# Optimization experiments

Hardware: AMD Instinct MI355X
Metric: run time of the kernel (lower is better)

The kernel has to match this reference:

```python
import jax, jax.numpy as jnp
import numpy as np

B, S, D = 4, 2048, 768
H = 12
HD = D // H  # 64
SCALE = HD ** -0.5

def setup_inputs() -> dict:
    key = jax.random.key(0)
    k1, k2, k3 = jax.random.split(key, 3)
    x = jax.random.normal(k1, (B, S, D), dtype=jnp.float32)
    w_qkv = jax.random.normal(k2, (D, 3 * D), dtype=jnp.float32) * (D ** -0.5)
    w_out = jax.random.normal(k3, (D, D), dtype=jnp.float32) * (D ** -0.5)
    b_out = jnp.zeros((D,), dtype=jnp.float32)
    return {"x": x, "w_qkv": w_qkv, "w_out": w_out, "b_out": b_out}

def reference(x, w_qkv, w_out, b_out):
    B_, S_, D_ = x.shape
    # qkv projection (no bias), then 'b s (qkv h d) -> qkv b h s d'
    qkv = (x @ w_qkv).reshape(B_, S_, 3, H, HD).transpose(2, 0, 3, 1, 4)
    q, k, v = qkv[0], qkv[1], qkv[2]  # each [B, H, S, HD]
    att = jnp.einsum('bhxd,bhyd->bhxy', q, k) * SCALE
    att = jax.nn.softmax(att, axis=-1)  # dropout_rate=0 -> identity
    out = jnp.einsum('bhxy,bhyd->bhxd', att, v)
    out = out.transpose(0, 2, 1, 3).reshape(B_, S_, D_)  # 'b h s d -> b s (h d)'
    return out @ w_out + b_out
```

## Files before the change

kernel.cpp:

```cpp
#include <hip/hip_runtime.h>

#define BB 4
#define SS 2048
#define DD 768
#define HH 12
#define HDIM 64

using bf16_t = __bf16;
typedef __bf16 bf16x8 __attribute__((ext_vector_type(8)));
typedef __bf16 bf16x4 __attribute__((ext_vector_type(4)));
typedef __bf16 bf16x2 __attribute__((ext_vector_type(2)));
typedef float f32x4 __attribute__((ext_vector_type(4)));
typedef float f32x16 __attribute__((ext_vector_type(16)));
typedef unsigned int u32;
typedef unsigned int u32x4 __attribute__((ext_vector_type(4)));

static __device__ __forceinline__ void cp16(void* lds, const void* g) {
  __builtin_amdgcn_global_load_lds(
      (const __attribute__((address_space(1))) u32*)g,
      (__attribute__((address_space(3))) u32*)lds, 16, 0, 0);
}

__global__ void cvt_x(const float* __restrict__ in, bf16_t* __restrict__ out) {
  const size_t i = ((size_t)blockIdx.x * 256 + threadIdx.x) * 8;
  f32x4 f0 = *(const f32x4*)(in + i);
  f32x4 f1 = *(const f32x4*)(in + i + 4);
  bf16x8 v;
#pragma unroll
  for (int j = 0; j < 4; j++) { v[j] = (bf16_t)f0[j]; v[4 + j] = (bf16_t)f1[j]; }
  *(bf16x8*)(out + i) = v;
}

__global__ void wt_transpose(const float* __restrict__ in, bf16_t* __restrict__ out,
                             int K, int N) {
  __shared__ bf16_t tile[64][65];
  const int n0 = blockIdx.x * 64, k0 = blockIdx.y * 64;
  const int t = threadIdx.x;
  const int r = t >> 2;
  const int c0 = (t & 3) * 16;
  const float* src = in + (size_t)(k0 + r) * N + n0 + c0;
#pragma unroll
  for (int q = 0; q < 4; q++) {
    f32x4 f = *(const f32x4*)(src + q * 4);
#pragma unroll
    for (int j = 0; j < 4; j++) tile[r][c0 + q * 4 + j] = (bf16_t)f[j];
  }
  __syncthreads();
  bf16x8 o0, o1;
#pragma unroll
  for (int j = 0; j < 8; j++) { o0[j] = tile[c0 + j][r]; o1[j] = tile[c0 + 8 + j][r]; }
  *(bf16x8*)(out + (size_t)(n0 + r) * K + k0 + c0) = o0;
  *(bf16x8*)(out + (size_t)(n0 + r) * K + k0 + c0 + 8) = o1;
}

template <int MODE>
__global__ __launch_bounds__(256, 2)
void gemm_bt(const bf16_t* __restrict__ A, const bf16_t* __restrict__ Bt,
             int M, int N, int K,
             bf16_t* __restrict__ q_out, bf16_t* __restrict__ k_out,
             bf16_t* __restrict__ vt_out,
             float* __restrict__ Cout, const float* __restrict__ bias) {
  __shared__ bf16_t As[2][128][64];
  __shared__ bf16_t Bs[2][128][64];
  const int t = threadIdx.x;
  const int lane = t & 63, wave = t >> 6;
  const int l15 = lane & 15, quad = lane >> 4;
  const int wm = (wave >> 1) * 64, wn = (wave & 1) * 64;

  const int nx = gridDim.x;
  const int L = blockIdx.y * nx + blockIdx.x;
  const int chunk = (nx * gridDim.y) >> 3;
  const int v = (L & 7) * chunk + (L >> 3);
  const int m0 = (v / nx) * 128, n0 = (v % nx) * 128;

  const int srow = lane >> 3;
  const int schunk = ((lane & 7) ^ srow) * 8;
  const int rsw = l15 & 7;

  f32x4 acc[4][4];
#pragma unroll
  for (int i = 0; i < 4; i++)
#pragma unroll
    for (int j = 0; j < 4; j++) acc[i][j] = (f32x4){0.f, 0.f, 0.f, 0.f};

  auto stage = [&](int k0, int buf) {
#pragma unroll
    for (int p = 0; p < 4; p++) {
      const int row = wave * 32 + p * 8 + srow;
      const bf16_t* asrc;
      if (MODE == 0) {
        asrc = A + (size_t)(m0 + row) * K + k0 + schunk;
      } else {
        const int mm = m0 + row, b = mm >> 11, s = mm & 2047, h = k0 >> 6;
        asrc = A + (((size_t)(b * HH + h)) * SS + s) * HDIM + schunk;
      }
      cp16(&As[buf][wave * 32 + p * 8][0], asrc);
      cp16(&Bs[buf][wave * 32 + p * 8][0],
           Bt + (size_t)(n0 + row) * K + k0 + schunk);
    }
  };

  const int NT = K / 64;
  stage(0, 0);

  for (int kt = 0; kt < NT; kt++) {
    const int buf = kt & 1;
    __syncthreads();
    if (kt + 1 < NT) stage((kt + 1) * 64, buf ^ 1);
#pragma unroll
    for (int kk = 0; kk < 2; kk++) {
      bf16x8 af[4], bfr[4];
#pragma unroll
      for (int i = 0; i < 4; i++)
        af[i] = *(const bf16x8*)&As[buf][wm + i * 16 + l15][((kk * 4 + quad) ^ rsw) * 8];
#pragma unroll
      for (int j = 0; j < 4; j++)
        bfr[j] = *(const bf16x8*)&Bs[buf][wn + j * 16 + l15][((kk * 4 + quad) ^ rsw) * 8];
#pragma unroll
      for (int i = 0; i < 4; i++)
#pragma unroll
        for (int j = 0; j < 4; j++)
          acc[i][j] = __builtin_amdgcn_mfma_f32_16x16x32_bf16(af[i], bfr[j], acc[i][j], 0, 0, 0);
    }
  }

  const float QSCALE = 0.125f * 1.44269504088896340736f;
#pragma unroll
  for (int i = 0; i < 4; i++) {
    const int mbase = m0 + wm + i * 16 + quad * 4;
#pragma unroll
    for (int j = 0; j < 4; j++) {
      const int n = n0 + wn + j * 16 + l15;
#pragma unroll
      for (int r = 0; r < 4; r++) {
        const float v = acc[i][j][r];
        const int mm = mbase + r;
        if (MODE == 0) {
          const int sel = n / DD;
          const int rem = n - sel * DD;
          const int h = rem >> 6, d = rem & 63;
          const int b = mm >> 11, s = mm & 2047;
          if (sel == 2) {
            vt_out[((size_t)(b * HH + h) * HDIM + d) * SS + s] = (bf16_t)v;
          } else {
            const size_t idx = (((size_t)(b * HH + h)) * SS + s) * HDIM + d;
            if (sel == 0) q_out[idx] = (bf16_t)(v * QSCALE);
            else k_out[idx] = (bf16_t)v;
          }
        } else {
          Cout[(size_t)mm * N + n] = v + bias[n];
        }
      }
    }
  }
}

__global__ __launch_bounds__(256, 3)
void attn_kernel(bf16_t* __restrict__ Qio, const bf16_t* __restrict__ Kg,
                 const bf16_t* __restrict__ Vt) {
  __shared__ bf16_t Ks[2][64][64];
  __shared__ bf16_t Vts[2][64][64];
  __shared__ float lsum[128];
  const int t = threadIdx.x;
  const int lane = t & 63, wave = t >> 6;
  const int l31 = lane & 31, hi = lane >> 5;

  const int L = blockIdx.y * gridDim.x + blockIdx.x;
  const int v = (L & 7) * ((16 * BB * HH) / 8) + (L >> 3);
  const int bh = v >> 4;
  const int q0 = (v & 15) * 128;

  const size_t base = (size_t)bh * SS * HDIM;
  const size_t baset = (size_t)bh * HDIM * SS;
  const int wq = wave * 32;
  const int srow = lane >> 3;
  const int schunk = ((lane & 7) ^ srow) * 8;
  const int rsw = l31 & 7;

  bf16x8 qf[4];
#pragma unroll
  for (int kd = 0; kd < 4; kd++)
    qf[kd] = *(const bf16x8*)(Qio + base + (size_t)(q0 + wq + l31) * HDIM +
                              kd * 16 + hi * 8);

  float l_lane = 0.f;
  f32x16 o_acc[2];
#pragma unroll
  for (int dt = 0; dt < 2; dt++)
#pragma unroll
    for (int r = 0; r < 16; r++) o_acc[dt][r] = 0.f;

  f32x16 sA[2], sB[2];

  auto stageK = [&](int k0, int buf) {
#pragma unroll
    for (int p = 0; p < 2; p++)
      cp16(&Ks[buf][wave * 16 + p * 8][0],
           Kg + base + (size_t)(k0 + wave * 16 + p * 8 + srow) * HDIM + schunk);
  };
  auto stageV = [&](int k0, int buf) {
#pragma unroll
    for (int p = 0; p < 2; p++)
      cp16(&Vts[buf][wave * 16 + p * 8][0],
           Vt + baset + (size_t)(wave * 16 + p * 8 + srow) * SS + k0 + schunk);
  };

  auto qk = [&](int buf, f32x16 (&s)[2]) {
    __builtin_amdgcn_s_setprio(1);
#pragma unroll
    for (int ct = 0; ct < 2; ct++) {
#pragma unroll
      for (int r = 0; r < 16; r++) s[ct][r] = 0.f;
#pragma unroll
      for (int kd = 0; kd < 4; kd++) {
        bf16x8 kf = *(const bf16x8*)&Ks[buf][ct * 32 + l31][((2 * kd + hi) ^ rsw) * 8];
        s[ct] = __builtin_amdgcn_mfma_f32_32x32x16_bf16(kf, qf[kd], s[ct], 0, 0, 0);
      }
    }
    __builtin_amdgcn_s_setprio(0);
  };

  auto smpv = [&](int buf, const f32x16 (&sT)[2]) {
    bf16x8 pa[4];
#pragma unroll
    for (int ct = 0; ct < 2; ct++) {
      float p[16];
#pragma unroll
      for (int r = 0; r < 16; r++) p[r] = __builtin_amdgcn_exp2f(sT[ct][r]);
#pragma unroll
      for (int r = 0; r < 16; r += 4)
        l_lane += (p[r] + p[r + 1]) + (p[r + 2] + p[r + 3]);
      u32 w[4][2];
#pragma unroll
      for (int g = 0; g < 4; g++)
#pragma unroll
        for (int i = 0; i < 2; i++) {
          bf16x2 pk = {(bf16_t)p[4 * g + 2 * i], (bf16_t)p[4 * g + 2 * i + 1]};
          w[g][i] = *(u32*)&pk;
        }
#pragma unroll
      for (int sub = 0; sub < 2; sub++) {
        u32 a0 = w[2 * sub][0], b0 = w[2 * sub + 1][0];
        u32 a1 = w[2 * sub][1], b1 = w[2 * sub + 1][1];
        asm volatile("v_permlane32_swap_b32 %0, %1" : "+v"(a0), "+v"(b0));
        asm volatile("v_permlane32_swap_b32 %0, %1" : "+v"(a1), "+v"(b1));
        u32x4 fr = {a0, a1, b0, b1};
        pa[ct * 2 + sub] = *(bf16x8*)&fr;
      }
    }
    __builtin_amdgcn_s_setprio(1);
#pragma unroll
    for (int kk = 0; kk < 4; kk++)
#pragma unroll
      for (int dt = 0; dt < 2; dt++) {
        bf16x8 vf = *(const bf16x8*)&Vts[buf][dt * 32 + l31][((2 * kk + hi) ^ rsw) * 8];
        o_acc[dt] = __builtin_amdgcn_mfma_f32_32x32x16_bf16(pa[kk], vf, o_acc[dt], 0, 0, 0);
      }
    __builtin_amdgcn_s_setprio(0);
  };

  stageK(0, 0); stageK(64, 1); stageV(0, 0);
  __syncthreads();
  qk(0, sA);
  __syncthreads();

#pragma unroll 1
  for (int it = 0; it < 30; it += 2) {
    stageK((it + 2) * 64, 0);
    stageV((it + 1) * 64, 1);
    qk(1, sB);
    smpv(0, sA);
    __syncthreads();
    stageK((it + 3) * 64, 1);
    stageV((it + 2) * 64, 0);
    qk(0, sA);
    smpv(1, sB);
    __syncthreads();
  }
  stageV(31 * 64, 1);
  qk(1, sB);
  smpv(0, sA);
  __syncthreads();
  smpv(1, sB);

  const float lf = l_lane + __shfl_xor(l_lane, 32);
  lsum[wq + l31] = lf;
#pragma unroll
  for (int r = 0; r < 16; r++) {
    const int q = wq + (r & 3) + 8 * (r >> 2) + 4 * hi;
    const float inv = 1.0f / lsum[q];
#pragma unroll
    for (int dt = 0; dt < 2; dt++) {
      const int d = dt * 32 + l31;
      Qio[base + (size_t)(q0 + q) * HDIM + d] = (bf16_t)(o_acc[dt][r] * inv);
    }
  }
}

extern "C" void kernel_launch(void* const* d_in, const int* in_sizes, int n_in,
                              void* d_out, int out_size, void* d_ws, size_t ws_size,
                              hipStream_t stream) {
  const float* x = (const float*)d_in[0];
  const float* w_qkv = (const float*)d_in[1];
  const float* w_out = (const float*)d_in[2];
  const float* b_out = (const float*)d_in[3];
  float* out = (float*)d_out;

  char* ws = (char*)d_ws;
  bf16_t* wqkv_t = (bf16_t*)ws; ws += (size_t)3 * DD * DD * 2;
  bf16_t* wout_t = (bf16_t*)ws; ws += (size_t)DD * DD * 2;
  bf16_t* q_ws = (bf16_t*)ws;   ws += (size_t)BB * HH * SS * HDIM * 2;
  bf16_t* k_ws = (bf16_t*)ws;
  bf16_t* vt_sc = (bf16_t*)d_out;
  bf16_t* xb = (bf16_t*)d_out + (size_t)BB * SS * DD;

  cvt_x<<<(BB * SS * DD) / (256 * 8), 256, 0, stream>>>(x, xb);
  wt_transpose<<<dim3(3 * DD / 64, DD / 64), 256, 0, stream>>>(w_qkv, wqkv_t, DD, 3 * DD);
  wt_transpose<<<dim3(DD / 64, DD / 64), 256, 0, stream>>>(w_out, wout_t, DD, DD);
  gemm_bt<0><<<dim3(3 * DD / 128, BB * SS / 128), 256, 0, stream>>>(
      xb, wqkv_t, BB * SS, 3 * DD, DD, q_ws, k_ws, vt_sc, nullptr, nullptr);
  attn_kernel<<<dim3(SS / 128, BB * HH), 256, 0, stream>>>(q_ws, k_ws, vt_sc);
  gemm_bt<1><<<dim3(DD / 128, BB * SS / 128), 256, 0, stream>>>(
      q_ws, wout_t, BB * SS, DD, DD, nullptr, nullptr, nullptr, out, b_out);
}
```

Baseline: 229.1 us.

## Halve GEMM K-tile to raise occupancy and change attention LDS swizzle

The GEMM kernel now stages 32-wide K slices instead of 64, halving LDS per block, and raises launch bounds so four blocks can fit per CU. The XOR swizzle on GEMM LDS reads is dropped, which may bring back bank conflicts, and the loop now does twice as many iterations and barriers. The attention kernel's K/V staging gets a different XOR swizzle that mixes in the row group, aimed at cutting LDS bank conflicts when the 32x32 MFMA fragments are read.

Result: slower. 246.2 us (+7.5%).

```diff
diff --git a/kernel.cpp b/kernel.cpp
--- a/kernel.cpp
+++ b/kernel.cpp
@@ -54,14 +54,14 @@
 }
 
 template <int MODE>
-__global__ __launch_bounds__(256, 2)
+__global__ __launch_bounds__(256, 4)
 void gemm_bt(const bf16_t* __restrict__ A, const bf16_t* __restrict__ Bt,
              int M, int N, int K,
              bf16_t* __restrict__ q_out, bf16_t* __restrict__ k_out,
              bf16_t* __restrict__ vt_out,
              float* __restrict__ Cout, const float* __restrict__ bias) {
-  __shared__ bf16_t As[2][128][64];
-  __shared__ bf16_t Bs[2][128][64];
+  __shared__ bf16_t As[2][128][32];
+  __shared__ bf16_t Bs[2][128][32];
   const int t = threadIdx.x;
   const int lane = t & 63, wave = t >> 6;
   const int l15 = lane & 15, quad = lane >> 4;
@@ -73,9 +73,8 @@
   const int v = (L & 7) * chunk + (L >> 3);
   const int m0 = (v / nx) * 128, n0 = (v % nx) * 128;
 
-  const int srow = lane >> 3;
-  const int schunk = ((lane & 7) ^ srow) * 8;
-  const int rsw = l15 & 7;
+  const int drow = lane >> 2;
+  const int dcol = (lane & 3) * 8;
 
   f32x4 acc[4][4];
 #pragma unroll
@@ -85,43 +84,40 @@
 
   auto stage = [&](int k0, int buf) {
 #pragma unroll
-    for (int p = 0; p < 4; p++) {
-      const int row = wave * 32 + p * 8 + srow;
+    for (int c = 0; c < 2; c++) {
+      const int row = wave * 32 + c * 16 + drow;
       const bf16_t* asrc;
       if (MODE == 0) {
-        asrc = A + (size_t)(m0 + row) * K + k0 + schunk;
+        asrc = A + (size_t)(m0 + row) * K + k0 + dcol;
       } else {
         const int mm = m0 + row, b = mm >> 11, s = mm & 2047, h = k0 >> 6;
-        asrc = A + (((size_t)(b * HH + h)) * SS + s) * HDIM + schunk;
-      }
-      cp16(&As[buf][wave * 32 + p * 8][0], asrc);
-      cp16(&Bs[buf][wave * 32 + p * 8][0],
-           Bt + (size_t)(n0 + row) * K + k0 + schunk);
-    }
-  };
-
-  const int NT = K / 64;
+        asrc = A + (((size_t)(b * HH + h)) * SS + s) * HDIM + (k0 & 63) + dcol;
+      }
+      cp16(&As[buf][wave * 32 + c * 16][0], asrc);
+      cp16(&Bs[buf][wave * 32 + c * 16][0],
+           Bt + (size_t)(n0 + row) * K + k0 + dcol);
+    }
+  };
+
+  const int NT = K / 32;
   stage(0, 0);
 
   for (int kt = 0; kt < NT; kt++) {
     const int buf = kt & 1;
     __syncthreads();
-    if (kt + 1 < NT) stage((kt + 1) * 64, buf ^ 1);
-#pragma unroll
-    for (int kk = 0; kk < 2; kk++) {
-      bf16x8 af[4], bfr[4];
-#pragma unroll
-      for (int i = 0; i < 4; i++)
-        af[i] = *(const bf16x8*)&As[buf][wm + i * 16 + l15][((kk * 4 + quad) ^ rsw) * 8];
+    if (kt + 1 < NT) stage((kt + 1) * 32, buf ^ 1);
+    bf16x8 af[4], bfr[4];
+#pragma unroll
+    for (int i = 0; i < 4; i++)
+      af[i] = *(const bf16x8*)&As[buf][wm + i * 16 + l15][quad * 8];
+#pragma unroll
+    for (int j = 0; j < 4; j++)
+      bfr[j] = *(const bf16x8*)&Bs[buf][wn + j * 16 + l15][quad * 8];
+#pragma unroll
+    for (int i = 0; i < 4; i++)
 #pragma unroll
       for (int j = 0; j < 4; j++)
-        bfr[j] = *(const bf16x8*)&Bs[buf][wn + j * 16 + l15][((kk * 4 + quad) ^ rsw) * 8];
-#pragma unroll
-      for (int i = 0; i < 4; i++)
-#pragma unroll
-        for (int j = 0; j < 4; j++)
-          acc[i][j] = __builtin_amdgcn_mfma_f32_16x16x32_bf16(af[i], bfr[j], acc[i][j], 0, 0, 0);
-    }
+        acc[i][j] = __builtin_amdgcn_mfma_f32_16x16x32_bf16(af[i], bfr[j], acc[i][j], 0, 0, 0);
   }
 
   const float QSCALE = 0.125f * 1.44269504088896340736f;
@@ -174,8 +170,7 @@
   const size_t baset = (size_t)bh * HDIM * SS;
   const int wq = wave * 32;
   const int srow = lane >> 3;
-  const int schunk = ((lane & 7) ^ srow) * 8;
-  const int rsw = l31 & 7;
+  const int rsw = (l31 & 7) ^ (l31 >> 3);
 
   bf16x8 qf[4];
 #pragma unroll
@@ -194,15 +189,19 @@
 
   auto stageK = [&](int k0, int buf) {
 #pragma unroll
-    for (int p = 0; p < 2; p++)
+    for (int p = 0; p < 2; p++) {
+      const int sc = ((lane & 7) ^ srow ^ ((wave * 2 + p) & 3)) * 8;
       cp16(&Ks[buf][wave * 16 + p * 8][0],
-           Kg + base + (size_t)(k0 + wave * 16 + p * 8 + srow) * HDIM + schunk);
+           Kg + base + (size_t)(k0 + wave * 16 + p * 8 + srow) * HDIM + sc);
+    }
   };
   auto stageV = [&](int k0, int buf) {
 #pragma unroll
-    for (int p = 0; p < 2; p++)
+    for (int p = 0; p < 2; p++) {
+      const int sc = ((lane & 7) ^ srow ^ ((wave * 2 + p) & 3)) * 8;
       cp16(&Vts[buf][wave * 16 + p * 8][0],
-           Vt + baset + (size_t)(wave * 16 + p * 8 + srow) * SS + k0 + schunk);
+           Vt + baset + (size_t)(wave * 16 + p * 8 + srow) * SS + k0 + sc);
+    }
   };
 
   auto qk = [&](int buf, f32x16 (&s)[2]) {
```

## Use 256x256 tiles for QKV GEMM and add extra LDS swizzle in attention

Applied to the files above, without the earlier changes.

Splits the templated GEMM into a dedicated QKV kernel using 256x256 output tiles, 512 threads and a K-step of 32, plus a separate projection kernel. The larger tile raises arithmetic intensity per LDS load and cuts the block count to 288. The attention kernel's K/V staging gets an extra XOR term in its swizzle, aimed at fewer LDS bank conflicts. In exchange, the larger accumulator raises register pressure, the shorter K-step means more barriers per unit of work, and fewer blocks may balance poorly across CUs.

After: 262.8 us. 14.7% more time.

```diff
diff --git a/kernel.cpp b/kernel.cpp
--- a/kernel.cpp
+++ b/kernel.cpp
@@ -53,19 +53,101 @@
   *(bf16x8*)(out + (size_t)(n0 + r) * K + k0 + c0 + 8) = o1;
 }
 
-template <int MODE>
+__global__ __launch_bounds__(512, 2)
+void gemm_qkv(const bf16_t* __restrict__ A, const bf16_t* __restrict__ Bt,
+              bf16_t* __restrict__ q_out, bf16_t* __restrict__ k_out,
+              bf16_t* __restrict__ vt_out) {
+  __shared__ bf16_t As[2][256][32];
+  __shared__ bf16_t Bs[2][256][32];
+  const int t = threadIdx.x;
+  const int lane = t & 63, wave = t >> 6;
+  const int l15 = lane & 15, quad = lane >> 4;
+  const int wm = (wave >> 2) * 128, wn = (wave & 3) * 64;
+  const int K = DD;
+
+  const int L = blockIdx.y * 9 + blockIdx.x;
+  const int v = (L & 7) * 36 + (L >> 3);
+  const int m0 = (v / 9) * 256, n0 = (v % 9) * 256;
+
+  const int drow = lane >> 2;
+  const int dcol = ((lane & 3) ^ ((lane >> 3) & 3)) * 8;
+  const int rxor = (l15 >> 1) & 3;
+
+  f32x4 acc[8][4];
+#pragma unroll
+  for (int i = 0; i < 8; i++)
+#pragma unroll
+    for (int j = 0; j < 4; j++) acc[i][j] = (f32x4){0.f, 0.f, 0.f, 0.f};
+
+  auto stage = [&](int k0, int buf) {
+#pragma unroll
+    for (int c = 0; c < 2; c++) {
+      const int row = wave * 32 + c * 16 + drow;
+      cp16(&As[buf][wave * 32 + c * 16][0],
+           A + (size_t)(m0 + row) * K + k0 + dcol);
+      cp16(&Bs[buf][wave * 32 + c * 16][0],
+           Bt + (size_t)(n0 + row) * K + k0 + dcol);
+    }
+  };
+
+  const int NT = K / 32;
+  stage(0, 0);
+
+  for (int kt = 0; kt < NT; kt++) {
+    const int buf = kt & 1;
+    __syncthreads();
+    if (kt + 1 < NT) stage((kt + 1) * 32, buf ^ 1);
+    bf16x8 af[8], bfr[4];
+#pragma unroll
+    for (int i = 0; i < 8; i++)
+      af[i] = *(const bf16x8*)&As[buf][wm + i * 16 + l15][(quad ^ rxor) * 8];
+#pragma unroll
+    for (int j = 0; j < 4; j++)
+      bfr[j] = *(const bf16x8*)&Bs[buf][wn + j * 16 + l15][(quad ^ rxor) * 8];
+#pragma unroll
+    for (int i = 0; i < 8; i++)
+#pragma unroll
+      for (int j = 0; j < 4; j++)
+        acc[i][j] = __builtin_amdgcn_mfma_f32_16x16x32_bf16(af[i], bfr[j], acc[i][j], 0, 0, 0);
+  }
+
+  const float QSCALE = 0.125f * 1.44269504088896340736f;
+#pragma unroll
+  for (int i = 0; i < 8; i++) {
+    const int mbase = m0 + wm + i * 16 + quad * 4;
+#pragma unroll
+    for (int j = 0; j < 4; j++) {
+      const int n = n0 + wn + j * 16 + l15;
+#pragma unroll
+      for (int r = 0; r < 4; r++) {
+        const float v = acc[i][j][r];
+        const int mm = mbase + r;
+        const int sel = n / DD;
+        const int rem = n - sel * DD;
+        const int h = rem >> 6, d = rem & 63;
+        const int b = mm >> 11, s = mm & 2047;
+        if (sel == 2) {
+          vt_out[((size_t)(b * HH + h) * HDIM + d) * SS + s] = (bf16_t)v;
+        } else {
+          const size_t idx = (((size_t)(b * HH + h)) * SS + s) * HDIM + d;
+          if (sel == 0) q_out[idx] = (bf16_t)(v * QSCALE);
+          else k_out[idx] = (bf16_t)v;
+        }
+      }
+    }
+  }
+}
+
 __global__ __launch_bounds__(256, 2)
-void gemm_bt(const bf16_t* __restrict__ A, const bf16_t* __restrict__ Bt,
-             int M, int N, int K,
-             bf16_t* __restrict__ q_out, bf16_t* __restrict__ k_out,
-             bf16_t* __restrict__ vt_out,
-             float* __restrict__ Cout, const float* __restrict__ bias) {
+void gemm_proj(const bf16_t* __restrict__ A, const bf16_t* __restrict__ Bt,
+               float* __restrict__ Cout, const float* __restrict__ bias) {
   __shared__ bf16_t As[2][128][64];
   __shared__ bf16_t Bs[2][128][64];
   const int t = threadIdx.x;
   const int lane = t & 63, wave = t >> 6;
   const int l15 = lane & 15, quad = lane >> 4;
   const int wm = (wave >> 1) * 64, wn = (wave & 1) * 64;
+  const int K = DD, N = DD;
 
   const int nx = gridDim.x;
   const int L = blockIdx.y * nx + blockIdx.x;
@@ -87,14 +169,9 @@
 #pragma unroll
     for (int p = 0; p < 4; p++) {
       const int row = wave * 32 + p * 8 + srow;
-      const bf16_t* asrc;
-      if (MODE == 0) {
-        asrc = A + (size_t)(m0 + row) * K + k0 + schunk;
-      } else {
-        const int mm = m0 + row, b = mm >> 11, s = mm & 2047, h = k0 >> 6;
-        asrc = A + (((size_t)(b * HH + h)) * SS + s) * HDIM + schunk;
-      }
-      cp16(&As[buf][wave * 32 + p * 8][0], asrc);
+      const int mm = m0 + row, b = mm >> 11, s = mm & 2047, h = k0 >> 6;
+      cp16(&As[buf][wave * 32 + p * 8][0],
+           A + (((size_t)(b * HH + h)) * SS + s) * HDIM + schunk);
       cp16(&Bs[buf][wave * 32 + p * 8][0],
            Bt + (size_t)(n0 + row) * K + k0 + schunk);
     }
@@ -124,7 +201,6 @@
     }
   }
 
-  const float QSCALE = 0.125f * 1.44269504088896340736f;
 #pragma unroll
   for (int i = 0; i < 4; i++) {
     const int mbase = m0 + wm + i * 16 + quad * 4;
@@ -132,25 +208,8 @@
     for (int j = 0; j < 4; j++) {
       const int n = n0 + wn + j * 16 + l15;
 #pragma unroll
-      for (int r = 0; r < 4; r++) {
-        const float v = acc[i][j][r];
-        const int mm = mbase + r;
-        if (MODE == 0) {
-          const int sel = n / DD;
-          const int rem = n - sel * DD;
-          const int h = rem >> 6, d = rem & 63;
-          const int b = mm >> 11, s = mm & 2047;
-          if (sel == 2) {
-            vt_out[((size_t)(b * HH + h) * HDIM + d) * SS + s] = (bf16_t)v;
-          } else {
-            const size_t idx = (((size_t)(b * HH + h)) * SS + s) * HDIM + d;
-            if (sel == 0) q_out[idx] = (bf16_t)(v * QSCALE);
-            else k_out[idx] = (bf16_t)v;
-          }
-        } else {
-          Cout[(size_t)mm * N + n] = v + bias[n];
-        }
-      }
+      for (int r = 0; r < 4; r++)
+        Cout[(size_t)(mbase + r) * N + n] = acc[i][j][r] + bias[n];
     }
   }
 }
@@ -174,8 +233,7 @@
   const size_t baset = (size_t)bh * HDIM * SS;
   const int wq = wave * 32;
   const int srow = lane >> 3;
-  const int schunk = ((lane & 7) ^ srow) * 8;
-  const int rsw = l31 & 7;
+  const int rsw = (l31 & 7) ^ (l31 >> 3);
 
   bf16x8 qf[4];
 #pragma unroll
@@ -194,15 +252,19 @@
 
   auto stageK = [&](int k0, int buf) {
 #pragma unroll
-    for (int p = 0; p < 2; p++)
+    for (int p = 0; p < 2; p++) {
+      const int sc = ((lane & 7) ^ srow ^ ((wave * 2 + p) & 3)) * 8;
       cp16(&Ks[buf][wave * 16 + p * 8][0],
-           Kg + base + (size_t)(k0 + wave * 16 + p * 8 + srow) * HDIM + schunk);
+           Kg + base + (size_t)(k0 + wave * 16 + p * 8 + srow) * HDIM + sc);
+    }
   };
   auto stageV = [&](int k0, int buf) {
 #pragma unroll
-    for (int p = 0; p < 2; p++)
+    for (int p = 0; p < 2; p++) {
+      const int sc = ((lane & 7) ^ srow ^ ((wave * 2 + p) & 3)) * 8;
       cp16(&Vts[buf][wave * 16 + p * 8][0],
-           Vt + baset + (size_t)(wave * 16 + p * 8 + srow) * SS + k0 + schunk);
+           Vt + baset + (size_t)(wave * 16 + p * 8 + srow) * SS + k0 + sc);
+    }
   };
 
   auto qk = [&](int buf, f32x16 (&s)[2]) {
@@ -317,9 +379,9 @@
   cvt_x<<<(BB * SS * DD) / (256 * 8), 256, 0, stream>>>(x, xb);
   wt_transpose<<<dim3(3 * DD / 64, DD / 64), 256, 0, stream>>>(w_qkv, wqkv_t, DD, 3 * DD);
   wt_transpose<<<dim3(DD / 64, DD / 64), 256, 0, stream>>>(w_out, wout_t, DD, DD);
-  gemm_bt<0><<<dim3(3 * DD / 128, BB * SS / 128), 256, 0, stream>>>(
-      xb, wqkv_t, BB * SS, 3 * DD, DD, q_ws, k_ws, vt_sc, nullptr, nullptr);
+  gemm_qkv<<<dim3((3 * DD) / 256, (BB * SS) / 256), 512, 0, stream>>>(
+      xb, wqkv_t, q_ws, k_ws, vt_sc);
   attn_kernel<<<dim3(SS / 128, BB * HH), 256, 0, stream>>>(q_ws, k_ws, vt_sc);
-  gemm_bt<1><<<dim3(DD / 128, BB * SS / 128), 256, 0, stream>>>(
-      q_ws, wout_t, BB * SS, DD, DD, nullptr, nullptr, nullptr, out, b_out);
-}
+  gemm_proj<<<dim3(DD / 128, (BB * SS) / 128), 256, 0, stream>>>(
+      q_ws, wout_t, out, b_out);
+}
```
